# Performance work log

Measured on AMD Instinct MI355X. Metric: run time of the kernel, lower is better.

The kernel has to match this reference:

```python
import jax, jax.numpy as jnp
import numpy as np

C_IN = 128
D_K = 256
D_V = 256
N_HEAD = 8
H = 192
W = 192
REGION = 3
TEMPER = int(np.sqrt(D_K))  # int(sqrt(d_k)) per the torch module


def setup_inputs() -> dict:
    key = jax.random.key(0)
    k1, k2, k3, k4 = jax.random.split(key, 4)
    scale = 1.0 / np.sqrt(C_IN).astype(np.float32)
    x = jax.random.normal(k1, (1, C_IN, H, W), dtype=jnp.float32)
    wq = jax.random.normal(k2, (D_K, C_IN), dtype=jnp.float32) * scale
    wk = jax.random.normal(k3, (D_K, C_IN), dtype=jnp.float32) * scale
    wv = jax.random.normal(k4, (D_V, C_IN), dtype=jnp.float32) * scale
    return {"x": x, "wq": wq, "wk": wk, "wv": wv}


def _stretch(t):
    # Equivalent of the fixed Conv3d 'stretch' trick: for each (i, j) in the
    # 3x3 region, channel 3*i+j holds the input shifted by (i-1, j-1), zero-padded.
    # t: [b, d, H, W] -> [b, 9, d, H, W]
    b, d, h, w = t.shape
    tp = jnp.pad(t, ((0, 0), (0, 0), (1, 1), (1, 1)))
    return jnp.stack(
        [tp[:, :, i:i + h, j:j + w] for i in range(REGION) for j in range(REGION)],
        axis=1,
    )


def reference(x, wq, wk, wv):
    b = x.shape[0]  # must be 1 (module's broadcast only works for batch 1)
    dkh = D_K // N_HEAD
    dvh = D_V // N_HEAD
    r2 = REGION * REGION
    # 1x1 conv projections == channel matmuls
    q = jnp.einsum('oc,bchw->bohw', wq, x)
    k = jnp.einsum('oc,bchw->bohw', wk, x)
    v = jnp.einsum('oc,bchw->bohw', wv, x)
    Q = _stretch(q)  # [b, 9, d_k, H, W]
    K = _stretch(k)
    V = _stretch(v)  # [b, 9, d_v, H, W]
    # elementwise QK, per-head channel sum, scale, softmax over the 9 region slots
    qk = (Q * K).reshape(b, r2, N_HEAD, dkh, H, W)
    scores = jax.nn.softmax(qk.sum(axis=3) / TEMPER, axis=1)  # [b, 9, n_head, H, W]
    # dropout is identity in eval mode (att_drop disabled for the reference)
    Vh = V.reshape(b, r2, N_HEAD, dvh, H, W)
    out = (scores[:, :, :, None] * Vh).sum(axis=1).reshape(b, D_V, H, W)
    return out
```

## Files before the change

kernel.cpp:

```cpp
#include <hip/hip_runtime.h>

#define HW_   36864
#define WI    192
#define HT    192
#define CIN   128
#define DK    256
#define NH    8
#define DKH   32

using short4_ = __attribute__((ext_vector_type(4))) short;
using short8  = __attribute__((ext_vector_type(8))) short;
using float4_ = __attribute__((ext_vector_type(4))) float;

static __device__ __forceinline__ float b2f(unsigned short u) {
    union { unsigned int i; float f; } x; x.i = ((unsigned int)u) << 16; return x.f;
}
static __device__ __forceinline__ unsigned short f2b(float f) {
    union { float f; unsigned int i; } x; x.f = f;
    unsigned int r = x.i + 0x7FFFu + ((x.i >> 16) & 1u);
    return (unsigned short)(r >> 16);
}

__global__ __launch_bounds__(256) void convw_kernel(
    const float* __restrict__ wq,
    const float* __restrict__ wk,
    const float* __restrict__ wv,
    unsigned short* __restrict__ wqkv)
{
    int id = blockIdx.x * 256 + threadIdx.x;
    int h   = id / 12288;
    int rem = id - h * 12288;
    int r   = rem >> 7;
    int c   = rem & 127;
    int g   = r >> 4;
    int gm  = g % 3;
    int rr  = ((g >= 3) ? 16 : 0) + (r & 15);
    const float* __restrict__ s = (gm == 0) ? wq : ((gm == 1) ? wk : wv);
    wqkv[id] = f2b(s[(h * 32 + rr) * 128 + c]);
}

__global__ __launch_bounds__(256) void projfused3_kernel(
    const float* __restrict__ x,
    const unsigned short* __restrict__ wqkv,
    unsigned short* __restrict__ vbuf,
    float* __restrict__ sbuf)
{
    __shared__ unsigned short ShA[2][96 * 136];
    __shared__ float sP[2][2][64];

    const int px0 = blockIdx.x * 64;
    const int t   = threadIdx.x;
    const int lane = t & 63, wave = t >> 6;
    const int col  = lane & 15, quad = lane >> 4;
    const int wm   = wave >> 1, wn = wave & 1;

    unsigned short* Bs = &ShA[0][0];
    #pragma unroll 4
    for (int i = 0; i < 32; ++i) {
        int id = i * 256 + t;
        int c = id >> 6, p = id & 63;
        Bs[p * 136 + c] = f2b(x[c * HW_ + px0 + p]);
    }
    __syncthreads();

    short8 bfrag[2][4];
    #pragma unroll
    for (int nt = 0; nt < 2; ++nt) {
        int n = wn * 32 + nt * 16 + col;
        #pragma unroll
        for (int kt = 0; kt < 4; ++kt)
            bfrag[nt][kt] = *(const short8*)&Bs[n * 136 + kt * 32 + quad * 8];
    }
    __syncthreads();

    {
        const unsigned short* __restrict__ Ag = wqkv;
        #pragma unroll
        for (int i = 0; i < 6; ++i) {
            int id = i * 256 + t;
            int row = id >> 4, c8 = id & 15;
            *(short8*)&ShA[0][row * 136 + c8 * 8] = *(const short8*)&Ag[row * 128 + c8 * 8];
        }
    }
    __syncthreads();

    for (int head = 0; head < 8; ++head) {
        if (head < 7) {
            const unsigned short* __restrict__ Ag = wqkv + (head + 1) * 96 * 128;
            unsigned short* __restrict__ Ad = &ShA[(head + 1) & 1][0];
            #pragma unroll
            for (int i = 0; i < 6; ++i) {
                int id = i * 256 + t;
                int row = id >> 4, c8 = id & 15;
                *(short8*)&Ad[row * 136 + c8 * 8] = *(const short8*)&Ag[row * 128 + c8 * 8];
            }
        }
        const unsigned short* __restrict__ As = &ShA[head & 1][0];

        float4_ acc[3][2];
        #pragma unroll
        for (int mt = 0; mt < 3; ++mt) {
            acc[mt][0] = (float4_){0.f, 0.f, 0.f, 0.f};
            acc[mt][1] = (float4_){0.f, 0.f, 0.f, 0.f};
        }

        #pragma unroll
        for (int mt = 0; mt < 3; ++mt) {
            #pragma unroll
            for (int kt = 0; kt < 4; ++kt) {
                short8 a = *(const short8*)&As[(wm * 48 + mt * 16 + col) * 136 + kt * 32 + quad * 8];
                acc[mt][0] = __builtin_amdgcn_mfma_f32_16x16x32_bf16(a, bfrag[0][kt], acc[mt][0], 0, 0, 0);
                acc[mt][1] = __builtin_amdgcn_mfma_f32_16x16x32_bf16(a, bfrag[1][kt], acc[mt][1], 0, 0, 0);
            }
        }

        #pragma unroll
        for (int nt = 0; nt < 2; ++nt) {
            int px = px0 + wn * 32 + nt * 16 + col;
            float s = 0.f;
            #pragma unroll
            for (int reg = 0; reg < 4; ++reg)
                s += acc[0][nt][reg] * acc[1][nt][reg];
            s += __shfl_xor(s, 16, 64);
            s += __shfl_xor(s, 32, 64);
            if (quad == 0) sP[head & 1][wm][wn * 32 + nt * 16 + col] = s;
            unsigned short* vp = vbuf + ((size_t)head * HW_ + px) * 32;
            short4_ v0;
            #pragma unroll
            for (int reg = 0; reg < 4; ++reg)
                v0[reg] = (short)f2b(acc[2][nt][reg]);
            *(short4_*)&vp[wm * 16 + quad * 4] = v0;
        }

        __syncthreads();

        if (t < 64)
            sbuf[head * HW_ + px0 + t] = sP[head & 1][0][t] + sP[head & 1][1][t];
    }
}

__global__ __launch_bounds__(256) void attn_kernel(
    const unsigned short* __restrict__ vbuf,
    const float* __restrict__ sbuf,
    float* __restrict__ out)
{
    __shared__ unsigned short Vh[6][18][32];
    __shared__ float Ssc[6][18];
    __shared__ float tr[32][65];

    const int b    = blockIdx.x;
    const int tile = b % 576;
    const int head = b / 576;
    const int t    = threadIdx.x;
    const int ty = tile / 12, tx = tile - ty * 12;
    const int y0 = ty * 4, x0 = tx * 16;

    const unsigned short* __restrict__ vb = vbuf + (size_t)head * HW_ * 32;
    const float* __restrict__ Sg = sbuf + head * HW_;

    for (int id = t; id < 432; id += 256) {
        int cell = id >> 2, q = id & 3;
        int hy = cell / 18, hx = cell - hy * 18;
        int gy = y0 - 1 + hy; gy = gy < 0 ? 0 : (gy > HT - 1 ? HT - 1 : gy);
        int gx = x0 - 1 + hx; gx = gx < 0 ? 0 : (gx > WI - 1 ? WI - 1 : gx);
        *(short8*)&Vh[hy][hx][q * 8] =
            *(const short8*)&vb[((size_t)(gy * WI + gx)) * 32 + q * 8];
    }
    if (t < 108) {
        int hy = t / 18, hx = t - hy * 18;
        int gy = y0 - 1 + hy; gy = gy < 0 ? 0 : (gy > HT - 1 ? HT - 1 : gy);
        int gx = x0 - 1 + hx; gx = gx < 0 ? 0 : (gx > WI - 1 ? WI - 1 : gx);
        Ssc[hy][hx] = Sg[gy * WI + gx];
    }
    __syncthreads();

    const int pxl = t >> 2;
    const int cg  = t & 3;
    const int ly  = pxl >> 4, lx = pxl & 15;
    const int y   = y0 + ly, xx = x0 + lx;

    float w[9];
    float m = -1e30f;
    #pragma unroll
    for (int r = 0; r < 9; ++r) {
        int dy = r / 3 - 1, dx = r % 3 - 1;
        int ny = y + dy, nx = xx + dx;
        bool inb = (ny >= 0) && (ny < HT) && (nx >= 0) && (nx < WI);
        float val = inb ? (Ssc[ly + dy + 1][lx + dx + 1] * 0.0625f) : 0.0f;
        w[r] = val;
        m = fmaxf(m, val);
    }
    float wsum = 0.f;
    #pragma unroll
    for (int r = 0; r < 9; ++r) {
        float e = __expf(w[r] - m);
        w[r] = e;
        wsum += e;
    }
    float inv = 1.0f / wsum;
    #pragma unroll
    for (int r = 0; r < 9; ++r) {
        int dy = r / 3 - 1, dx = r % 3 - 1;
        int ny = y + dy, nx = xx + dx;
        bool inb = (ny >= 0) && (ny < HT) && (nx >= 0) && (nx < WI);
        w[r] = inb ? (w[r] * inv) : 0.0f;
    }

    float acc[8] = {0.f, 0.f, 0.f, 0.f, 0.f, 0.f, 0.f, 0.f};
    #pragma unroll
    for (int r = 0; r < 9; ++r) {
        int dy = r / 3 - 1, dx = r % 3 - 1;
        short8 v8 = *(const short8*)&Vh[ly + dy + 1][lx + dx + 1][cg * 8];
        #pragma unroll
        for (int j = 0; j < 8; ++j)
            acc[j] = fmaf(w[r], b2f((unsigned short)v8[j]), acc[j]);
    }
    #pragma unroll
    for (int j = 0; j < 8; ++j)
        tr[cg * 8 + j][pxl] = acc[j];
    __syncthreads();

    const int ch   = t >> 3;
    const int ly2  = (t >> 1) & 3;
    const int half = t & 1;
    float4_ o0, o1;
    #pragma unroll
    for (int j = 0; j < 4; ++j) {
        o0[j] = tr[ch][ly2 * 16 + half * 8 + j];
        o1[j] = tr[ch][ly2 * 16 + half * 8 + 4 + j];
    }
    float* o = out + (size_t)(head * DKH + ch) * HW_ + (y0 + ly2) * WI + x0 + half * 8;
    *(float4_*)&o[0] = o0;
    *(float4_*)&o[4] = o1;
}

extern "C" void kernel_launch(void* const* d_in, const int* in_sizes, int n_in,
                              void* d_out, int out_size, void* d_ws, size_t ws_size,
                              hipStream_t stream) {
    const float* x  = (const float*)d_in[0];
    const float* wq = (const float*)d_in[1];
    const float* wk = (const float*)d_in[2];
    const float* wv = (const float*)d_in[3];

    char* ws = (char*)d_ws;
    unsigned short* wqkv = (unsigned short*)ws;
    unsigned short* vbuf = (unsigned short*)(ws + 196608);
    float*          sbuf = (float*)(ws + 19071104);

    convw_kernel<<<384, 256, 0, stream>>>(wq, wk, wv, wqkv);
    projfused3_kernel<<<576, 256, 0, stream>>>(x, wqkv, vbuf, sbuf);
    attn_kernel<<<4608, 256, 0, stream>>>(vbuf, sbuf, (float*)d_out);
}
```

Measured before the change: 109.2 us.

## Enlarge attention tile to 8x16 pixels and interleave heads across blocks

The attention kernel now covers an 8-row by 16-column tile per block instead of 4 rows, so the one-pixel halo in the staged V and score buffers is a smaller share of each load. Block count is halved. Each thread now handles 16 channels of one pixel instead of 8, and the output transpose runs in two halves through the same shared buffer. Blocks are remapped so consecutive block IDs cycle across heads (b&7 picks the head), which may spread concurrent work differently across XCDs and caches. The cost is more registers per thread, an extra barrier, and fewer blocks available to hide latency.

```diff
diff --git a/kernel.cpp b/kernel.cpp
--- a/kernel.cpp
+++ b/kernel.cpp
@@ -144,21 +144,22 @@
     const float* __restrict__ sbuf,
     float* __restrict__ out)
 {
-    __shared__ unsigned short Vh[6][18][32];
-    __shared__ float Ssc[6][18];
+    __shared__ unsigned short Vh[10][18][32];
+    __shared__ float Ssc[10][18];
     __shared__ float tr[32][65];
 
     const int b    = blockIdx.x;
-    const int tile = b % 576;
-    const int head = b / 576;
+    const int wg   = (b & 7) * 288 + (b >> 3);
+    const int head = wg / 288;
+    const int tile = wg - head * 288;
     const int t    = threadIdx.x;
     const int ty = tile / 12, tx = tile - ty * 12;
-    const int y0 = ty * 4, x0 = tx * 16;
+    const int y0 = ty * 8, x0 = tx * 16;
 
     const unsigned short* __restrict__ vb = vbuf + (size_t)head * HW_ * 32;
     const float* __restrict__ Sg = sbuf + head * HW_;
 
-    for (int id = t; id < 432; id += 256) {
+    for (int id = t; id < 720; id += 256) {
         int cell = id >> 2, q = id & 3;
         int hy = cell / 18, hx = cell - hy * 18;
         int gy = y0 - 1 + hy; gy = gy < 0 ? 0 : (gy > HT - 1 ? HT - 1 : gy);
@@ -166,7 +167,7 @@
         *(short8*)&Vh[hy][hx][q * 8] =
             *(const short8*)&vb[((size_t)(gy * WI + gx)) * 32 + q * 8];
     }
-    if (t < 108) {
+    if (t < 180) {
         int hy = t / 18, hx = t - hy * 18;
         int gy = y0 - 1 + hy; gy = gy < 0 ? 0 : (gy > HT - 1 ? HT - 1 : gy);
         int gx = x0 - 1 + hx; gx = gx < 0 ? 0 : (gx > WI - 1 ? WI - 1 : gx);
@@ -174,8 +175,8 @@
     }
     __syncthreads();
 
-    const int pxl = t >> 2;
-    const int cg  = t & 3;
+    const int pxl = t >> 1;
+    const int hg  = t & 1;
     const int ly  = pxl >> 4, lx = pxl & 15;
     const int y   = y0 + ly, xx = x0 + lx;
 
@@ -206,32 +207,45 @@
         w[r] = inb ? (w[r] * inv) : 0.0f;
     }
 
-    float acc[8] = {0.f, 0.f, 0.f, 0.f, 0.f, 0.f, 0.f, 0.f};
+    float acc[16];
+    #pragma unroll
+    for (int j = 0; j < 16; ++j) acc[j] = 0.f;
     #pragma unroll
     for (int r = 0; r < 9; ++r) {
         int dy = r / 3 - 1, dx = r % 3 - 1;
-        short8 v8 = *(const short8*)&Vh[ly + dy + 1][lx + dx + 1][cg * 8];
-        #pragma unroll
-        for (int j = 0; j < 8; ++j)
-            acc[j] = fmaf(w[r], b2f((unsigned short)v8[j]), acc[j]);
-    }
-    #pragma unroll
-    for (int j = 0; j < 8; ++j)
-        tr[cg * 8 + j][pxl] = acc[j];
-    __syncthreads();
-
-    const int ch   = t >> 3;
-    const int ly2  = (t >> 1) & 3;
-    const int half = t & 1;
-    float4_ o0, o1;
-    #pragma unroll
-    for (int j = 0; j < 4; ++j) {
-        o0[j] = tr[ch][ly2 * 16 + half * 8 + j];
-        o1[j] = tr[ch][ly2 * 16 + half * 8 + 4 + j];
-    }
-    float* o = out + (size_t)(head * DKH + ch) * HW_ + (y0 + ly2) * WI + x0 + half * 8;
-    *(float4_*)&o[0] = o0;
-    *(float4_*)&o[4] = o1;
+        const unsigned short* vp = &Vh[ly + dy + 1][lx + dx + 1][hg * 16];
+        short8 v8a = *(const short8*)&vp[0];
+        short8 v8b = *(const short8*)&vp[8];
+        #pragma unroll
+        for (int j = 0; j < 8; ++j) {
+            acc[j]     = fmaf(w[r], b2f((unsigned short)v8a[j]), acc[j]);
+            acc[8 + j] = fmaf(w[r], b2f((unsigned short)v8b[j]), acc[8 + j]);
+        }
+    }
+
+    const int ch  = t >> 3;
+    const int sub = t & 7;
+    const int ly2 = sub >> 1, xh = sub & 1;
+    #pragma unroll
+    for (int h = 0; h < 2; ++h) {
+        if (h) __syncthreads();
+        if ((pxl >> 6) == h) {
+            #pragma unroll
+            for (int j = 0; j < 16; ++j)
+                tr[hg * 16 + j][pxl & 63] = acc[j];
+        }
+        __syncthreads();
+        float4_ o0, o1;
+        #pragma unroll
+        for (int j = 0; j < 4; ++j) {
+            o0[j] = tr[ch][ly2 * 16 + xh * 8 + j];
+            o1[j] = tr[ch][ly2 * 16 + xh * 8 + 4 + j];
+        }
+        float* o = out + (size_t)(head * DKH + ch) * HW_
+                 + (y0 + h * 4 + ly2) * WI + x0 + xh * 8;
+        *(float4_*)&o[0] = o0;
+        *(float4_*)&o[4] = o1;
+    }
 }
 
 extern "C" void kernel_launch(void* const* d_in, const int* in_sizes, int n_in,
@@ -249,5 +263,5 @@
 
     convw_kernel<<<384, 256, 0, stream>>>(wq, wk, wv, wqkv);
     projfused3_kernel<<<576, 256, 0, stream>>>(x, wqkv, vbuf, sbuf);
-    attn_kernel<<<4608, 256, 0, stream>>>(vbuf, sbuf, (float*)d_out);
-}
+    attn_kernel<<<2304, 256, 0, stream>>>(vbuf, sbuf, (float*)d_out);
+}
```

Result: no change. 109.3 us, median of 2 (+0.1%).
